# Kernel optimization log

Measured on AMD Instinct MI355X. Metric: run time of the kernel, lower is better.

Reference implementation:

```python
import jax, jax.numpy as jnp
import numpy as np

N, IN_F, OUT_F, K = 256, 1024, 128, 32

def setup_inputs() -> dict:
    key = jax.random.key(0)
    k1, k2 = jax.random.split(key)
    x = jax.random.normal(k1, (N, IN_F), dtype=jnp.float32)
    T = jax.random.normal(k2, (IN_F, OUT_F, K), dtype=jnp.float32)
    return {"x": x, "T": T}

def reference(x, T):
    # matrices: [N, OUT_F, K]
    M = jnp.einsum('ni,iok->nok', x, T)
    # pairwise L1 distance over kernel dim: [N, N, OUT_F]
    norm = jnp.abs(M[:, None, :, :] - M[None, :, :, :]).sum(axis=3)
    expnorm = jnp.exp(-norm)
    # sum over the other-sample axis; subtract self-term exp(0)=1
    o_b = expnorm.sum(axis=0) - 1.0  # [N, OUT_F]
    return jnp.concatenate([x, o_b], axis=1)
```

## Files before the change

kernel.cpp:

```cpp
#include <hip/hip_runtime.h>

typedef unsigned short u16;
typedef __attribute__((ext_vector_type(8))) short short8_t;
typedef __attribute__((ext_vector_type(4))) float f32x4;

#define N_SAMP 256
#define IN_F   1024
#define OUT_F  128
#define KDIM   32
#define JTOT   (OUT_F * KDIM)
#define OUT_ROW (IN_F + OUT_F)
#define MT_ELEMS ((size_t)JTOT * N_SAMP)

#define CHUNKS 8
#define MPC    32
#define MPW    8

__device__ __forceinline__ u16 f2bf(float f) {
    union { float f; unsigned u; } v; v.f = f;
    unsigned r = v.u + 0x7FFFu + ((v.u >> 16) & 1u);
    return (u16)(r >> 16);
}


#define LDB 136
__global__ __launch_bounds__(256) void gemm_fused(const float* __restrict__ x,
                                                  const float* __restrict__ T,
                                                  float* __restrict__ out,
                                                  float* __restrict__ Mt) {
    __shared__ u16 Bs[2][64 * LDB];
    __shared__ u16 As[2][64 * LDB];
    const int t = threadIdx.x, w = t >> 6, l = t & 63;
    const int wr = (w >> 1) * 32, wc = (w & 1) * 32;
    const int jb = blockIdx.x * 64, nb = blockIdx.y * 64;
    const int kbase = blockIdx.z * 512;
    float* Mth = Mt + (size_t)blockIdx.z * MT_ELEMS;

    if (blockIdx.z == 0 && blockIdx.x < 16) {
        const int row = nb + blockIdx.x * 4 + (t >> 6);
        const float4* src = reinterpret_cast<const float4*>(x + (size_t)row * IN_F);
        float4* dst = reinterpret_cast<float4*>(out + (size_t)row * OUT_ROW);
#pragma unroll
        for (int i = 0; i < 4; ++i) dst[(t & 63) + 64 * i] = src[(t & 63) + 64 * i];
    }

    const int kp = t >> 2;
    const int q  = t & 3;

    f32x4 acc00 = {0.f,0.f,0.f,0.f}, acc01 = {0.f,0.f,0.f,0.f};
    f32x4 acc10 = {0.f,0.f,0.f,0.f}, acc11 = {0.f,0.f,0.f,0.f};

    float4 ta[4], tb[4], xv[8];
    auto LOADG = [&](int it) {
        const int k0 = kbase + it * 128;
        const float4* gT0 = reinterpret_cast<const float4*>(T + (size_t)(k0 + 2 * kp    ) * JTOT + jb + q * 16);
        const float4* gT1 = reinterpret_cast<const float4*>(T + (size_t)(k0 + 2 * kp + 1) * JTOT + jb + q * 16);
#pragma unroll
        for (int i = 0; i < 4; ++i) { ta[i] = gT0[i]; tb[i] = gT1[i]; }
        const float4* gx = reinterpret_cast<const float4*>(x + (size_t)(nb + kp) * IN_F + k0 + q * 32);
#pragma unroll
        for (int i = 0; i < 8; ++i) xv[i] = gx[i];
    };
    auto STORE = [&](int b) {
#pragma unroll
        for (int i = 0; i < 4; ++i) {
            const float* fa = reinterpret_cast<const float*>(&ta[i]);
            const float* fb = reinterpret_cast<const float*>(&tb[i]);
#pragma unroll
            for (int c = 0; c < 4; ++c) {
                unsigned v = (unsigned)f2bf(fa[c]) | ((unsigned)f2bf(fb[c]) << 16);
                *reinterpret_cast<unsigned*>(&Bs[b][(q * 16 + i * 4 + c) * LDB + 2 * kp]) = v;
            }
        }
#pragma unroll
        for (int i = 0; i < 4; ++i) {
            const float* f0 = reinterpret_cast<const float*>(&xv[2 * i]);
            const float* f1 = reinterpret_cast<const float*>(&xv[2 * i + 1]);
            uint4 pv;
            pv.x = (unsigned)f2bf(f0[0]) | ((unsigned)f2bf(f0[1]) << 16);
            pv.y = (unsigned)f2bf(f0[2]) | ((unsigned)f2bf(f0[3]) << 16);
            pv.z = (unsigned)f2bf(f1[0]) | ((unsigned)f2bf(f1[1]) << 16);
            pv.w = (unsigned)f2bf(f1[2]) | ((unsigned)f2bf(f1[3]) << 16);
            *reinterpret_cast<uint4*>(&As[b][kp * LDB + q * 32 + i * 8]) = pv;
        }
    };

    LOADG(0); STORE(0); __syncthreads();

    for (int it = 0; it < 4; ++it) {
        const int cur = it & 1;
        if (it < 3) LOADG(it + 1);
#pragma unroll
        for (int s = 0; s < 4; ++s) {
            const int co = s * 32 + 8 * (l >> 4);
            short8_t a0 = *reinterpret_cast<const short8_t*>(&Bs[cur][(wr +      (l & 15)) * LDB + co]);
            short8_t a1 = *reinterpret_cast<const short8_t*>(&Bs[cur][(wr + 16 + (l & 15)) * LDB + co]);
            short8_t b0 = *reinterpret_cast<const short8_t*>(&As[cur][(wc +      (l & 15)) * LDB + co]);
            short8_t b1 = *reinterpret_cast<const short8_t*>(&As[cur][(wc + 16 + (l & 15)) * LDB + co]);
            acc00 = __builtin_amdgcn_mfma_f32_16x16x32_bf16(a0, b0, acc00, 0, 0, 0);
            acc01 = __builtin_amdgcn_mfma_f32_16x16x32_bf16(a0, b1, acc01, 0, 0, 0);
            acc10 = __builtin_amdgcn_mfma_f32_16x16x32_bf16(a1, b0, acc10, 0, 0, 0);
            acc11 = __builtin_amdgcn_mfma_f32_16x16x32_bf16(a1, b1, acc11, 0, 0, 0);
        }
        if (it < 3) STORE(cur ^ 1);
        __syncthreads();
    }

    const int jrow = jb + wr + (l >> 4) * 4;
    const int ncol = nb + wc + (l & 15);
#pragma unroll
    for (int r = 0; r < 4; ++r) {
        Mth[(size_t)(jrow + r     ) * N_SAMP + ncol     ] = acc00[r];
        Mth[(size_t)(jrow + r     ) * N_SAMP + ncol + 16] = acc01[r];
        Mth[(size_t)(jrow + 16 + r) * N_SAMP + ncol     ] = acc10[r];
        Mth[(size_t)(jrow + 16 + r) * N_SAMP + ncol + 16] = acc11[r];
    }
}

__global__ __launch_bounds__(256) void dist_part(const float* __restrict__ Mt,
                                                 float* __restrict__ part) {
    __shared__ float Mo[MPC][36];
    __shared__ float Pred[4][N_SAMP];
    const int t = threadIdx.x, w = t >> 6, l = t & 63;
    const int o  = blockIdx.x;
    const int mb = blockIdx.y * MPC;
    const float* Mt1 = Mt + MT_ELEMS;

    {
        const int m = t & 31, kb = (t >> 5) * 4;
#pragma unroll
        for (int kk = 0; kk < 4; ++kk) {
            size_t idx = (size_t)(o * KDIM + kb + kk) * N_SAMP + mb + m;
            Mo[m][kb + kk] = Mt[idx] + Mt1[idx];
        }
    }
    __syncthreads();

    float accd[4][MPW];
#pragma unroll
    for (int r = 0; r < 4; ++r)
#pragma unroll
        for (int m = 0; m < MPW; ++m) accd[r][m] = 0.f;

#pragma unroll
    for (int kh = 0; kh < 4; ++kh) {
        float r0[8], r1[8], r2[8], r3[8];
#pragma unroll
        for (int k = 0; k < 8; ++k) {
            const size_t off = (size_t)(o * KDIM + kh * 8 + k) * N_SAMP + l;
            const float* p0 = Mt  + off;
            const float* p1 = Mt1 + off;
            r0[k] = p0[0]   + p1[0];
            r1[k] = p0[64]  + p1[64];
            r2[k] = p0[128] + p1[128];
            r3[k] = p0[192] + p1[192];
        }
#pragma unroll
        for (int m = 0; m < MPW; ++m) {
            float mo[8];
#pragma unroll
            for (int i = 0; i < 2; ++i)
                *reinterpret_cast<float4*>(&mo[i * 4]) =
                    *reinterpret_cast<const float4*>(&Mo[w * MPW + m][kh * 8 + i * 4]);
#pragma unroll
            for (int k = 0; k < 8; ++k) {
                accd[0][m] += fabsf(r0[k] - mo[k]);
                accd[1][m] += fabsf(r1[k] - mo[k]);
                accd[2][m] += fabsf(r2[k] - mo[k]);
                accd[3][m] += fabsf(r3[k] - mo[k]);
            }
        }
    }

    float a0 = 0.f, a1 = 0.f, a2 = 0.f, a3 = 0.f;
#pragma unroll
    for (int m = 0; m < MPW; ++m) {
        a0 += __expf(-accd[0][m]); a1 += __expf(-accd[1][m]);
        a2 += __expf(-accd[2][m]); a3 += __expf(-accd[3][m]);
    }
    Pred[w][l] = a0; Pred[w][l + 64] = a1; Pred[w][l + 128] = a2; Pred[w][l + 192] = a3;
    __syncthreads();

    {
        float s = Pred[0][t] + Pred[1][t] + Pred[2][t] + Pred[3][t];
        part[(size_t)blockIdx.y * (OUT_F * N_SAMP) + o * N_SAMP + t] = s;
    }
}

__global__ __launch_bounds__(256) void dist_reduce(const float* __restrict__ part,
                                                   float* __restrict__ out) {
    const int o = blockIdx.x, n = threadIdx.x;
    float s = -1.0f;
#pragma unroll
    for (int c = 0; c < CHUNKS; ++c)
        s += part[(size_t)c * (OUT_F * N_SAMP) + o * N_SAMP + n];
    out[(size_t)n * OUT_ROW + IN_F + o] = s;
}

__global__ __launch_bounds__(256) void copy_init_kernel(const float* __restrict__ x,
                                                        float* __restrict__ out) {
    int n = blockIdx.x, t = threadIdx.x;
    reinterpret_cast<float4*>(out + (size_t)n * OUT_ROW)[t] =
        reinterpret_cast<const float4*>(x + (size_t)n * IN_F)[t];
    if (t < OUT_F) out[(size_t)n * OUT_ROW + IN_F + t] = -1.0f;
}

#define BM 64
#define BN 64
#define BK 16
#define AS_STRIDE 68
__global__ __launch_bounds__(256) void gemm_kernel(const float* __restrict__ x,
                                                   const float* __restrict__ T,
                                                   float* __restrict__ M) {
    __shared__ float As_[BK][AS_STRIDE];
    __shared__ float Bs_[BK][BN];
    const int jb = blockIdx.x * BN, nb = blockIdx.y * BM;
    const int t = threadIdx.x, tx = t & 15, ty = t >> 4;
    float acc[4][4] = {};
    for (int k0 = 0; k0 < IN_F; k0 += BK) {
        {
            int row = t >> 2, cg = (t & 3) * 4;
            float4 v = *reinterpret_cast<const float4*>(&x[(size_t)(nb + row) * IN_F + k0 + cg]);
            As_[cg + 0][row] = v.x; As_[cg + 1][row] = v.y;
            As_[cg + 2][row] = v.z; As_[cg + 3][row] = v.w;
        }
        {
            int r = t >> 4, cg = (t & 15) * 4;
            *reinterpret_cast<float4*>(&Bs_[r][cg]) =
                *reinterpret_cast<const float4*>(&T[(size_t)(k0 + r) * JTOT + jb + cg]);
        }
        __syncthreads();
#pragma unroll
        for (int kk = 0; kk < BK; ++kk) {
            float4 av = *reinterpret_cast<const float4*>(&As_[kk][ty * 4]);
            float4 bv = *reinterpret_cast<const float4*>(&Bs_[kk][tx * 4]);
            float a[4] = {av.x, av.y, av.z, av.w}, b[4] = {bv.x, bv.y, bv.z, bv.w};
#pragma unroll
            for (int i = 0; i < 4; ++i)
#pragma unroll
                for (int j = 0; j < 4; ++j) acc[i][j] += a[i] * b[j];
        }
        __syncthreads();
    }
#pragma unroll
    for (int i = 0; i < 4; ++i) {
        int n = nb + ty * 4 + i;
        float4 v = make_float4(acc[i][0], acc[i][1], acc[i][2], acc[i][3]);
        *reinterpret_cast<float4*>(&M[(size_t)n * JTOT + jb + tx * 4]) = v;
    }
}

__global__ __launch_bounds__(256) void dist_kernel(const float* __restrict__ M,
                                                   float* __restrict__ out) {
    __shared__ float Mo_[64][KDIM];
    const int o = blockIdx.x >> 2, chunk = blockIdx.x & 3, t = threadIdx.x;
    float r[KDIM];
    const float4* mrow = reinterpret_cast<const float4*>(&M[(size_t)t * JTOT + o * KDIM]);
#pragma unroll
    for (int f = 0; f < 8; ++f) {
        float4 v = mrow[f];
        r[f*4+0]=v.x; r[f*4+1]=v.y; r[f*4+2]=v.z; r[f*4+3]=v.w;
    }
    const int mbase = chunk * 64;
    {
        int row = t >> 3, f4 = t & 7;
        *reinterpret_cast<float4*>(&Mo_[row][f4*4]) =
            *reinterpret_cast<const float4*>(&M[(size_t)(mbase+row)*JTOT + o*KDIM + f4*4]);
        *reinterpret_cast<float4*>(&Mo_[row+32][f4*4]) =
            *reinterpret_cast<const float4*>(&M[(size_t)(mbase+row+32)*JTOT + o*KDIM + f4*4]);
    }
    __syncthreads();
    float acc = 0.f;
    for (int m = 0; m < 64; ++m) {
        float d = 0.f;
#pragma unroll
        for (int k = 0; k < KDIM; ++k) d += fabsf(r[k] - Mo_[m][k]);
        acc += __expf(-d);
    }
    atomicAdd(&out[(size_t)t * OUT_ROW + IN_F + o], acc);
}

extern "C" void kernel_launch(void* const* d_in, const int* in_sizes, int n_in,
                              void* d_out, int out_size, void* d_ws, size_t ws_size,
                              hipStream_t stream) {
    const float* x = (const float*)d_in[0];
    const float* T = (const float*)d_in[1];
    float* out = (float*)d_out;

    const size_t NEED = 2 * MT_ELEMS * 4 + (size_t)CHUNKS * OUT_F * N_SAMP * 4;

    if (ws_size >= NEED) {
        float* Mt   = (float*)d_ws;
        float* part = Mt + 2 * MT_ELEMS;

        gemm_fused<<<dim3(JTOT / 64, N_SAMP / 64, 2), 256, 0, stream>>>(x, T, out, Mt);
        dist_part<<<dim3(OUT_F, CHUNKS), 256, 0, stream>>>(Mt, part);
        dist_reduce<<<OUT_F, 256, 0, stream>>>(part, out);
    } else {
        float* M = (float*)d_ws;
        copy_init_kernel<<<N_SAMP, 256, 0, stream>>>(x, out);
        dim3 ggrid(JTOT / BN, N_SAMP / BM);
        gemm_kernel<<<ggrid, 256, 0, stream>>>(x, T, M);
        dist_kernel<<<OUT_F * 4, 256, 0, stream>>>(M, out);
    }
}
```

Before: 103.4 us.

## Restructure GEMM to full-N tiles with 4-way split-K and separate partial-sum kernel

The GEMM now has each 512-thread block cover all 256 samples for a 64-column slice of T, with 4-way split-K instead of 2-way, so each T element is loaded once rather than once per 64-sample tile. A new sum_halves kernel adds the four partial M buffers into one, and dist_part now reads that single summed buffer instead of adding two partials on the fly. This cuts redundant global reads of T and the repeated partial-sum adds in the distance kernel. The cost is an extra kernel launch, more workspace, and extra traffic to write and read the four partial buffers.

```diff
diff --git a/kernel.cpp b/kernel.cpp
--- a/kernel.cpp
+++ b/kernel.cpp
@@ -12,6 +12,12 @@
 #define OUT_ROW (IN_F + OUT_F)
 #define MT_ELEMS ((size_t)JTOT * N_SAMP)
 
+#define NKZ    4
+#define KPERKZ (IN_F / NKZ)
+#define KSTEP  64
+#define NSTEPS (KPERKZ / KSTEP)
+#define LDB2   72
+
 #define CHUNKS 8
 #define MPC    32
 #define MPW    8
@@ -21,100 +27,121 @@
     unsigned r = v.u + 0x7FFFu + ((v.u >> 16) & 1u);
     return (u16)(r >> 16);
 }
-
-
-#define LDB 136
-__global__ __launch_bounds__(256) void gemm_fused(const float* __restrict__ x,
-                                                  const float* __restrict__ T,
-                                                  float* __restrict__ out,
-                                                  float* __restrict__ Mt) {
-    __shared__ u16 Bs[2][64 * LDB];
-    __shared__ u16 As[2][64 * LDB];
+__device__ __forceinline__ unsigned pack2(float lo, float hi) {
+    return (unsigned)f2bf(lo) | ((unsigned)f2bf(hi) << 16);
+}
+
+
+__global__ __launch_bounds__(512) void gemm_fused2(const float* __restrict__ x,
+                                                   const float* __restrict__ T,
+                                                   float* __restrict__ out,
+                                                   float* __restrict__ Mt) {
+    __shared__ u16 Bs[2][64 * LDB2];
+    __shared__ u16 As[2][256 * LDB2];
     const int t = threadIdx.x, w = t >> 6, l = t & 63;
-    const int wr = (w >> 1) * 32, wc = (w & 1) * 32;
-    const int jb = blockIdx.x * 64, nb = blockIdx.y * 64;
-    const int kbase = blockIdx.z * 512;
-    float* Mth = Mt + (size_t)blockIdx.z * MT_ELEMS;
-
-    if (blockIdx.z == 0 && blockIdx.x < 16) {
-        const int row = nb + blockIdx.x * 4 + (t >> 6);
+    const int wj = w >> 2, wn = w & 3;
+    const int jb = blockIdx.x * 64;
+    const int kz = blockIdx.y, kbase = kz * KPERKZ;
+    float* Mth = Mt + (size_t)kz * MT_ELEMS;
+
+    if (kz == 0) {
+        const int row = blockIdx.x * 4 + (t >> 7);
+        const int c  = t & 127;
         const float4* src = reinterpret_cast<const float4*>(x + (size_t)row * IN_F);
         float4* dst = reinterpret_cast<float4*>(out + (size_t)row * OUT_ROW);
-#pragma unroll
-        for (int i = 0; i < 4; ++i) dst[(t & 63) + 64 * i] = src[(t & 63) + 64 * i];
-    }
-
-    const int kp = t >> 2;
-    const int q  = t & 3;
-
-    f32x4 acc00 = {0.f,0.f,0.f,0.f}, acc01 = {0.f,0.f,0.f,0.f};
-    f32x4 acc10 = {0.f,0.f,0.f,0.f}, acc11 = {0.f,0.f,0.f,0.f};
-
-    float4 ta[4], tb[4], xv[8];
+        dst[c] = src[c];
+        dst[c + 128] = src[c + 128];
+    }
+
+    const int tj  = t & 15;
+    const int tk4 = (t >> 4) * 4;
+    const int xn  = t >> 1;
+    const int xh  = t & 1;
+
+    f32x4 acc[2][4];
+#pragma unroll
+    for (int a = 0; a < 2; ++a)
+#pragma unroll
+        for (int b = 0; b < 4; ++b) acc[a][b] = (f32x4){0.f, 0.f, 0.f, 0.f};
+
+    float4 ta[4], xv[8];
     auto LOADG = [&](int it) {
-        const int k0 = kbase + it * 128;
-        const float4* gT0 = reinterpret_cast<const float4*>(T + (size_t)(k0 + 2 * kp    ) * JTOT + jb + q * 16);
-        const float4* gT1 = reinterpret_cast<const float4*>(T + (size_t)(k0 + 2 * kp + 1) * JTOT + jb + q * 16);
-#pragma unroll
-        for (int i = 0; i < 4; ++i) { ta[i] = gT0[i]; tb[i] = gT1[i]; }
-        const float4* gx = reinterpret_cast<const float4*>(x + (size_t)(nb + kp) * IN_F + k0 + q * 32);
-#pragma unroll
-        for (int i = 0; i < 8; ++i) xv[i] = gx[i];
+        const int k0 = kbase + it * KSTEP;
+        if (t < 256) {
+#pragma unroll
+            for (int r = 0; r < 4; ++r)
+                ta[r] = *reinterpret_cast<const float4*>(&T[(size_t)(k0 + tk4 + r) * JTOT + jb + tj * 4]);
+        }
+#pragma unroll
+        for (int i = 0; i < 8; ++i)
+            xv[i] = *reinterpret_cast<const float4*>(&x[(size_t)xn * IN_F + k0 + xh * 32 + i * 4]);
     };
-    auto STORE = [&](int b) {
+    auto STOREB = [&](int b) {
+        if (t < 256) {
+            const float* f0 = reinterpret_cast<const float*>(&ta[0]);
+            const float* f1 = reinterpret_cast<const float*>(&ta[1]);
+            const float* f2 = reinterpret_cast<const float*>(&ta[2]);
+            const float* f3 = reinterpret_cast<const float*>(&ta[3]);
+#pragma unroll
+            for (int c = 0; c < 4; ++c) {
+                uint2 pv = make_uint2(pack2(f0[c], f1[c]), pack2(f2[c], f3[c]));
+                *reinterpret_cast<uint2*>(&Bs[b][(tj * 4 + c) * LDB2 + tk4]) = pv;
+            }
+        }
 #pragma unroll
         for (int i = 0; i < 4; ++i) {
-            const float* fa = reinterpret_cast<const float*>(&ta[i]);
-            const float* fb = reinterpret_cast<const float*>(&tb[i]);
-#pragma unroll
-            for (int c = 0; c < 4; ++c) {
-                unsigned v = (unsigned)f2bf(fa[c]) | ((unsigned)f2bf(fb[c]) << 16);
-                *reinterpret_cast<unsigned*>(&Bs[b][(q * 16 + i * 4 + c) * LDB + 2 * kp]) = v;
+            const float* g0 = reinterpret_cast<const float*>(&xv[2 * i]);
+            const float* g1 = reinterpret_cast<const float*>(&xv[2 * i + 1]);
+            uint4 pv = make_uint4(pack2(g0[0], g0[1]), pack2(g0[2], g0[3]),
+                                  pack2(g1[0], g1[1]), pack2(g1[2], g1[3]));
+            *reinterpret_cast<uint4*>(&As[b][xn * LDB2 + xh * 32 + i * 8]) = pv;
+        }
+    };
+
+    LOADG(0); STOREB(0); __syncthreads();
+
+    for (int it = 0; it < NSTEPS; ++it) {
+        const int cur = it & 1;
+        if (it < NSTEPS - 1) LOADG(it + 1);
+#pragma unroll
+        for (int s = 0; s < 2; ++s) {
+            const int co = s * 32 + 8 * (l >> 4);
+            short8_t a0 = *reinterpret_cast<const short8_t*>(&Bs[cur][(wj * 32 +      (l & 15)) * LDB2 + co]);
+            short8_t a1 = *reinterpret_cast<const short8_t*>(&Bs[cur][(wj * 32 + 16 + (l & 15)) * LDB2 + co]);
+#pragma unroll
+            for (int ni = 0; ni < 4; ++ni) {
+                short8_t bn = *reinterpret_cast<const short8_t*>(&As[cur][(wn * 64 + ni * 16 + (l & 15)) * LDB2 + co]);
+                acc[0][ni] = __builtin_amdgcn_mfma_f32_16x16x32_bf16(a0, bn, acc[0][ni], 0, 0, 0);
+                acc[1][ni] = __builtin_amdgcn_mfma_f32_16x16x32_bf16(a1, bn, acc[1][ni], 0, 0, 0);
             }
         }
-#pragma unroll
-        for (int i = 0; i < 4; ++i) {
-            const float* f0 = reinterpret_cast<const float*>(&xv[2 * i]);
-            const float* f1 = reinterpret_cast<const float*>(&xv[2 * i + 1]);
-            uint4 pv;
-            pv.x = (unsigned)f2bf(f0[0]) | ((unsigned)f2bf(f0[1]) << 16);
-            pv.y = (unsigned)f2bf(f0[2]) | ((unsigned)f2bf(f0[3]) << 16);
-            pv.z = (unsigned)f2bf(f1[0]) | ((unsigned)f2bf(f1[1]) << 16);
-            pv.w = (unsigned)f2bf(f1[2]) | ((unsigned)f2bf(f1[3]) << 16);
-            *reinterpret_cast<uint4*>(&As[b][kp * LDB + q * 32 + i * 8]) = pv;
-        }
-    };
-
-    LOADG(0); STORE(0); __syncthreads();
-
-    for (int it = 0; it < 4; ++it) {
-        const int cur = it & 1;
-        if (it < 3) LOADG(it + 1);
-#pragma unroll
-        for (int s = 0; s < 4; ++s) {
-            const int co = s * 32 + 8 * (l >> 4);
-            short8_t a0 = *reinterpret_cast<const short8_t*>(&Bs[cur][(wr +      (l & 15)) * LDB + co]);
-            short8_t a1 = *reinterpret_cast<const short8_t*>(&Bs[cur][(wr + 16 + (l & 15)) * LDB + co]);
-            short8_t b0 = *reinterpret_cast<const short8_t*>(&As[cur][(wc +      (l & 15)) * LDB + co]);
-            short8_t b1 = *reinterpret_cast<const short8_t*>(&As[cur][(wc + 16 + (l & 15)) * LDB + co]);
-            acc00 = __builtin_amdgcn_mfma_f32_16x16x32_bf16(a0, b0, acc00, 0, 0, 0);
-            acc01 = __builtin_amdgcn_mfma_f32_16x16x32_bf16(a0, b1, acc01, 0, 0, 0);
-            acc10 = __builtin_amdgcn_mfma_f32_16x16x32_bf16(a1, b0, acc10, 0, 0, 0);
-            acc11 = __builtin_amdgcn_mfma_f32_16x16x32_bf16(a1, b1, acc11, 0, 0, 0);
-        }
-        if (it < 3) STORE(cur ^ 1);
+        if (it < NSTEPS - 1) STOREB(cur ^ 1);
         __syncthreads();
     }
 
-    const int jrow = jb + wr + (l >> 4) * 4;
-    const int ncol = nb + wc + (l & 15);
-#pragma unroll
-    for (int r = 0; r < 4; ++r) {
-        Mth[(size_t)(jrow + r     ) * N_SAMP + ncol     ] = acc00[r];
-        Mth[(size_t)(jrow + r     ) * N_SAMP + ncol + 16] = acc01[r];
-        Mth[(size_t)(jrow + 16 + r) * N_SAMP + ncol     ] = acc10[r];
-        Mth[(size_t)(jrow + 16 + r) * N_SAMP + ncol + 16] = acc11[r];
-    }
+    const int jrow = jb + wj * 32 + (l >> 4) * 4;
+#pragma unroll
+    for (int ni = 0; ni < 4; ++ni) {
+        const int ncol = wn * 64 + ni * 16 + (l & 15);
+#pragma unroll
+        for (int r = 0; r < 4; ++r) {
+            Mth[(size_t)(jrow + r     ) * N_SAMP + ncol] = acc[0][ni][r];
+            Mth[(size_t)(jrow + 16 + r) * N_SAMP + ncol] = acc[1][ni][r];
+        }
+    }
+}
+
+__global__ __launch_bounds__(256) void sum_halves(const float* __restrict__ Mt,
+                                                  float* __restrict__ Mtsum) {
+    const size_t i = (size_t)blockIdx.x * 256 + threadIdx.x;
+    const float4* h0 = reinterpret_cast<const float4*>(Mt);
+    const float4* h1 = h0 + MT_ELEMS / 4;
+    const float4* h2 = h1 + MT_ELEMS / 4;
+    const float4* h3 = h2 + MT_ELEMS / 4;
+    float4 a = h0[i], b = h1[i], c = h2[i], d = h3[i];
+    float4 s = make_float4(a.x + b.x + c.x + d.x, a.y + b.y + c.y + d.y,
+                           a.z + b.z + c.z + d.z, a.w + b.w + c.w + d.w);
+    reinterpret_cast<float4*>(Mtsum)[i] = s;
 }
 
 __global__ __launch_bounds__(256) void dist_part(const float* __restrict__ Mt,
@@ -124,15 +151,12 @@
     const int t = threadIdx.x, w = t >> 6, l = t & 63;
     const int o  = blockIdx.x;
     const int mb = blockIdx.y * MPC;
-    const float* Mt1 = Mt + MT_ELEMS;
 
     {
         const int m = t & 31, kb = (t >> 5) * 4;
 #pragma unroll
-        for (int kk = 0; kk < 4; ++kk) {
-            size_t idx = (size_t)(o * KDIM + kb + kk) * N_SAMP + mb + m;
-            Mo[m][kb + kk] = Mt[idx] + Mt1[idx];
-        }
+        for (int kk = 0; kk < 4; ++kk)
+            Mo[m][kb + kk] = Mt[(size_t)(o * KDIM + kb + kk) * N_SAMP + mb + m];
     }
     __syncthreads();
 
@@ -147,13 +171,8 @@
         float r0[8], r1[8], r2[8], r3[8];
 #pragma unroll
         for (int k = 0; k < 8; ++k) {
-            const size_t off = (size_t)(o * KDIM + kh * 8 + k) * N_SAMP + l;
-            const float* p0 = Mt  + off;
-            const float* p1 = Mt1 + off;
-            r0[k] = p0[0]   + p1[0];
-            r1[k] = p0[64]  + p1[64];
-            r2[k] = p0[128] + p1[128];
-            r3[k] = p0[192] + p1[192];
+            const float* p = Mt + (size_t)(o * KDIM + kh * 8 + k) * N_SAMP + l;
+            r0[k] = p[0]; r1[k] = p[64]; r2[k] = p[128]; r3[k] = p[192];
         }
 #pragma unroll
         for (int m = 0; m < MPW; ++m) {
@@ -287,14 +306,16 @@
     const float* T = (const float*)d_in[1];
     float* out = (float*)d_out;
 
-    const size_t NEED = 2 * MT_ELEMS * 4 + (size_t)CHUNKS * OUT_F * N_SAMP * 4;
+    const size_t NEED = (NKZ + 1) * MT_ELEMS * 4 + (size_t)CHUNKS * OUT_F * N_SAMP * 4;
 
     if (ws_size >= NEED) {
-        float* Mt   = (float*)d_ws;
-        float* part = Mt + 2 * MT_ELEMS;
-
-        gemm_fused<<<dim3(JTOT / 64, N_SAMP / 64, 2), 256, 0, stream>>>(x, T, out, Mt);
-        dist_part<<<dim3(OUT_F, CHUNKS), 256, 0, stream>>>(Mt, part);
+        float* Mt    = (float*)d_ws;
+        float* Mtsum = Mt + (size_t)NKZ * MT_ELEMS;
+        float* part  = Mtsum + MT_ELEMS;
+
+        gemm_fused2<<<dim3(JTOT / 64, NKZ), 512, 0, stream>>>(x, T, out, Mt);
+        sum_halves<<<MT_ELEMS / 4 / 256, 256, 0, stream>>>(Mt, Mtsum);
+        dist_part<<<dim3(OUT_F, CHUNKS), 256, 0, stream>>>(Mtsum, part);
         dist_reduce<<<OUT_F, 256, 0, stream>>>(part, out);
     } else {
         float* M = (float*)d_ws;
```

Result: faster. 97.33 us (-5.8%).
